# Kernel tuning notes

Hardware: AMD Instinct MI355X
Metric: run time of the kernel (lower is better)

## Reference

```python
import jax, jax.numpy as jnp
import numpy as np

# Module config (matches init_kwargs)
DIM = 1024
NUM_HEADS = 16
HEAD_DIM = DIM // NUM_HEADS
SCALE = HEAD_DIM ** -0.5
WINDOW = 256
EXT = WINDOW // 2  # overlap_window=True -> ext_size = window_size // 2

B, N = 4, 4096  # N is a multiple of WINDOW


def setup_inputs() -> dict:
    key = jax.random.key(0)
    ks = jax.random.split(key, 5)
    x = jax.random.normal(ks[0], (B, N, DIM), dtype=jnp.float32)
    # Learned params (trunc-normal std=0.02 in torch; plain normal*0.02 is fine as a stand-in)
    w_qkv = jax.random.normal(ks[1], (3 * DIM, DIM), dtype=jnp.float32) * 0.02
    b_qkv = jnp.zeros((3 * DIM,), dtype=jnp.float32)
    w_proj = jax.random.normal(ks[2], (DIM, DIM), dtype=jnp.float32) * 0.02
    b_proj = jnp.zeros((DIM,), dtype=jnp.float32)
    return {"x": x, "w_qkv": w_qkv, "b_qkv": b_qkv, "w_proj": w_proj, "b_proj": b_proj}


def _local_attention(x, w_qkv, b_qkv, w_proj, b_proj):
    b, n, c = x.shape
    h, hd, w, e = NUM_HEADS, HEAD_DIM, WINDOW, EXT
    g = n // w  # number of windows (n is a multiple of w)
    kw_len = w + 2 * e  # extended window length for keys/values

    # qkv projection and head split: (3, b, h, n, hd)
    qkv = (x @ w_qkv.T + b_qkv).reshape(b, n, 3, h, hd).transpose(2, 0, 3, 1, 4)
    q, k, v = qkv[0], qkv[1], qkv[2]

    # q: non-overlapping windows -> (b, h, g, w, hd)
    qw = q.reshape(b, h, g, w, hd)

    # k, v: pad seq by ext on both sides, then strided overlapping windows
    kp = jnp.pad(k, ((0, 0), (0, 0), (e, e), (0, 0)))
    vp = jnp.pad(v, ((0, 0), (0, 0), (e, e), (0, 0)))
    # window g covers padded positions [g*w, g*w + kw_len)
    idx = jnp.arange(g)[:, None] * w + jnp.arange(kw_len)[None, :]  # (g, kw_len)
    kw = kp[:, :, idx]  # (b, h, g, kw_len, hd)
    vw = vp[:, :, idx]

    # per-window attention
    dots = jnp.einsum('bhgqd,bhgkd->bhgqk', qw, kw) * SCALE  # (b, h, g, w, kw_len)
    # mask out keys that came from the ext padding (out of [0, n) range)
    pos = idx - e  # global key positions per window
    valid = (pos >= 0) & (pos < n)  # (g, kw_len)
    dots = jnp.where(valid[None, None, :, None, :], dots, -jnp.inf)
    attn = jax.nn.softmax(dots, axis=-1)
    out = jnp.einsum('bhgqk,bhgkd->bhgqd', attn, vw)  # (b, h, g, w, hd)

    # merge windows and heads: (b, n, c)
    out = out.reshape(b, h, n, hd).transpose(0, 2, 1, 3).reshape(b, n, c)
    return out @ w_proj.T + b_proj


def reference(x, w_qkv, b_qkv, w_proj, b_proj):
    return _local_attention(x, w_qkv, b_qkv, w_proj, b_proj)
```

## Files before the change

### kernel.cpp

```cpp
#include <hip/hip_runtime.h>


typedef __attribute__((ext_vector_type(8))) short short8;
typedef __attribute__((ext_vector_type(4))) float f32x4;
typedef __attribute__((ext_vector_type(8))) unsigned short ushort8v;
typedef __attribute__((ext_vector_type(4))) unsigned short ushort4v;
typedef __attribute__((ext_vector_type(4))) unsigned int uint4v;
typedef __attribute__((ext_vector_type(4))) _Float16 half4;

#define K_DIM 1024

__device__ __forceinline__ unsigned short f2bf(float f) {
  unsigned int u = __builtin_bit_cast(unsigned int, f);
  u += 0x7FFFu + ((u >> 16) & 1u);
  return (unsigned short)(u >> 16);
}
__device__ __forceinline__ unsigned short f2h(float f) {
  _Float16 h = (_Float16)f;
  return __builtin_bit_cast(unsigned short, h);
}
__device__ __forceinline__ void gload_lds(const unsigned short* g, unsigned short* l) {
  __builtin_amdgcn_global_load_lds((const __attribute__((address_space(1))) void*)g,
                                   (__attribute__((address_space(3))) void*)l, 16, 0, 0);
}

__global__ __launch_bounds__(256) void convf2b(const float* __restrict__ src,
                                               unsigned short* __restrict__ dst, int n4) {
  int i = blockIdx.x * blockDim.x + threadIdx.x;
  if (i >= n4) return;
  f32x4 v = *(const f32x4*)(src + (size_t)i * 4);
  ushort4v o;
  o[0] = f2bf(v[0]); o[1] = f2bf(v[1]); o[2] = f2bf(v[2]); o[3] = f2bf(v[3]);
  *(ushort4v*)(dst + (size_t)i * 4) = o;
}

__device__ __forceinline__ void gemm_core(const unsigned short* __restrict__ A,
                                          const unsigned short* __restrict__ Bw,
                                          unsigned short* As, unsigned short* Bs,
                                          int m0, int f0, int tid, f32x4 acc[4][4]) {
  const int lane = tid & 63;
  const int w = tid >> 6;
  const int wm = (tid >> 7) & 1;
  const int wn = (tid >> 6) & 1;
  const int q15 = lane & 15, quad = lane >> 4;
  const int sw = q15 & 3;
  for (int kk = 0; kk < K_DIM; kk += 32) {
#pragma unroll
    for (int r = 0; r < 2; ++r) {
      int c = tid + r * 256;
      int row = c >> 2, s = c & 3;
      int gs = s ^ (row & 3);
      const unsigned short* ga = A + (size_t)(m0 + row) * K_DIM + kk + gs * 8;
      const unsigned short* gb = Bw + (size_t)(f0 + row) * K_DIM + kk + gs * 8;
      unsigned short* la = As + (size_t)(w * 64 + r * 256) * 8;
      unsigned short* lb = Bs + (size_t)(w * 64 + r * 256) * 8;
      gload_lds(ga, la);
      gload_lds(gb, lb);
    }
    __syncthreads();
    short8 af[4], bf[4];
#pragma unroll
    for (int i = 0; i < 4; ++i)
      af[i] = *(const short8*)&As[(wm * 64 + i * 16 + q15) * 32 + (quad ^ sw) * 8];
#pragma unroll
    for (int j = 0; j < 4; ++j)
      bf[j] = *(const short8*)&Bs[(wn * 64 + j * 16 + q15) * 32 + (quad ^ sw) * 8];
#pragma unroll
    for (int i = 0; i < 4; ++i)
#pragma unroll
      for (int j = 0; j < 4; ++j)
        acc[i][j] = __builtin_amdgcn_mfma_f32_16x16x32_bf16(af[i], bf[j], acc[i][j], 0, 0, 0);
    __syncthreads();
  }
}

__global__ __launch_bounds__(256) void gemm_qkv(const unsigned short* __restrict__ A,
                                                const unsigned short* __restrict__ Bw,
                                                const float* __restrict__ bias,
                                                unsigned short* __restrict__ q,
                                                unsigned short* __restrict__ k,
                                                unsigned short* __restrict__ v) {
  __shared__ unsigned short As[128 * 32];
  __shared__ unsigned short Bs[128 * 32];
  int m0 = (blockIdx.x & 127) * 128;
  int f0 = (blockIdx.x >> 7) * 128;
  int tid = threadIdx.x;
  f32x4 acc[4][4] = {};
  gemm_core(A, Bw, As, Bs, m0, f0, tid, acc);
  int lane = tid & 63;
  int wm = (tid >> 7) & 1, wn = (tid >> 6) & 1;
  int which = f0 >> 10;
  unsigned short* dst = (which == 0) ? q : ((which == 1) ? k : v);
#pragma unroll
  for (int j = 0; j < 4; ++j) {
    int f = f0 + wn * 64 + j * 16 + (lane & 15);
    int hh = (f >> 6) & 15;
    int d = f & 63;
    float bj = bias[f];
#pragma unroll
    for (int i = 0; i < 4; ++i) {
#pragma unroll
      for (int r = 0; r < 4; ++r) {
        int m = m0 + wm * 64 + i * 16 + (lane >> 4) * 4 + r;
        int bb = m >> 12, n = m & 4095;
        float val = acc[i][j][r] + bj;
        dst[((size_t)(bb * 16 + hh) * 4096 + n) * 64 + d] =
            (which == 2) ? f2h(val) : f2bf(val);
      }
    }
  }
}

__global__ __launch_bounds__(256) void gemm_proj(const unsigned short* __restrict__ A,
                                                 const unsigned short* __restrict__ Bw,
                                                 const float* __restrict__ bias,
                                                 float* __restrict__ out) {
  __shared__ unsigned short As[128 * 32];
  __shared__ unsigned short Bs[128 * 32];
  int m0 = (blockIdx.x & 127) * 128;
  int f0 = (blockIdx.x >> 7) * 128;
  int tid = threadIdx.x;
  f32x4 acc[4][4] = {};
  gemm_core(A, Bw, As, Bs, m0, f0, tid, acc);
  int lane = tid & 63;
  int wm = (tid >> 7) & 1, wn = (tid >> 6) & 1;
#pragma unroll
  for (int j = 0; j < 4; ++j) {
    int f = f0 + wn * 64 + j * 16 + (lane & 15);
    float bj = bias[f];
#pragma unroll
    for (int i = 0; i < 4; ++i) {
#pragma unroll
      for (int r = 0; r < 4; ++r) {
        int m = m0 + wm * 64 + i * 16 + (lane >> 4) * 4 + r;
        out[(size_t)m * 1024 + f] = acc[i][j][r] + bj;
      }
    }
  }
}

__global__ __launch_bounds__(256) void transpose_v(const unsigned short* __restrict__ v,
                                                   unsigned short* __restrict__ vt) {
  __shared__ unsigned short tile[64][72];
  int bid = blockIdx.x;
  int bh = bid >> 6;
  int n0 = (bid & 63) * 64;
  int tid = threadIdx.x;
#pragma unroll
  for (int r = 0; r < 2; ++r) {
    int c = tid + r * 256;
    int row = c >> 3, col8 = (c & 7) * 8;
    uint4v dv = *(const uint4v*)&v[((size_t)bh * 4096 + n0 + row) * 64 + col8];
    *(uint4v*)&tile[row][col8] = dv;
  }
  __syncthreads();
#pragma unroll
  for (int r = 0; r < 2; ++r) {
    int c = tid + r * 256;
    int d = c >> 3, n8 = (c & 7) * 8;
    ushort8v o;
#pragma unroll
    for (int ii = 0; ii < 8; ++ii) o[ii] = tile[n8 + ii][d];
    *(ushort8v*)&vt[((size_t)bh * 64 + d) * 4096 + n0 + n8] = o;
  }
}

__global__ __launch_bounds__(256) void attn3(const unsigned short* __restrict__ Q,
                                             const unsigned short* __restrict__ Kb,
                                             const unsigned short* __restrict__ Vt,
                                             unsigned short* __restrict__ Ao) {
  __shared__ unsigned short lds2[2][8192];

  int bid = blockIdx.x;
  int qb = bid & 63;
  int bh = bid >> 6;
  int b = bh >> 4, h = bh & 15;
  int tid = threadIdx.x, lane = tid & 63, w = tid >> 6;
  int q0 = qb * 64 + w * 16;
  int g = qb >> 2;
  int kst = g * 256 - 128;
  const size_t base = (size_t)bh * 4096 * 64;
  const int q15 = lane & 15, quad = lane >> 4;

  short8 bq[2];
#pragma unroll
  for (int s = 0; s < 2; ++s)
    bq[s] = *(const short8*)&Q[base + (size_t)(q0 + q15) * 64 + s * 32 + quad * 8];

  half4 spk[32];
  float mx = -1e30f;

  auto stageK = [&](int c, int buf) {
    int kb = kst + c * 128;
    kb = min(max(kb, 0), 4096 - 128);
    const unsigned short* Kg = Kb + base + (size_t)kb * 64;
#pragma unroll
    for (int i = 0; i < 4; ++i) {
      int slot = tid + i * 256;
      int row = slot >> 3, s = slot & 7;
      int gs = s ^ (row & 7);
      gload_lds(Kg + (size_t)row * 64 + gs * 8, &lds2[buf][(w * 64 + i * 256) * 8]);
    }
  };

  stageK(0, 0);
#pragma unroll
  for (int c = 0; c < 4; ++c) {
    __syncthreads();
    if (c < 3) stageK(c + 1, (c + 1) & 1);
    const unsigned short* Kc = lds2[c & 1];
    int r7 = q15 & 7;
#pragma unroll
    for (int nt = 0; nt < 8; ++nt) {
      int t = c * 8 + nt;
      int ky = kst + c * 128 + nt * 16;
      bool valid = (ky >= 0) && (ky < 4096);
      if (valid) {
        int sg0 = quad ^ r7;
        const unsigned short* kr = &Kc[(nt * 16 + q15) * 64];
        short8 ak0 = *(const short8*)&kr[sg0 * 8];
        short8 ak1 = *(const short8*)&kr[(sg0 ^ 4) * 8];
        f32x4 sa = {0.f, 0.f, 0.f, 0.f};
        sa = __builtin_amdgcn_mfma_f32_16x16x32_bf16(ak0, bq[0], sa, 0, 0, 0);
        sa = __builtin_amdgcn_mfma_f32_16x16x32_bf16(ak1, bq[1], sa, 0, 0, 0);
        float s0 = sa[0] * 0.125f, s1 = sa[1] * 0.125f;
        float s2 = sa[2] * 0.125f, s3 = sa[3] * 0.125f;
        mx = fmaxf(mx, fmaxf(fmaxf(s0, s1), fmaxf(s2, s3)));
        half4 pk;
        pk[0] = (_Float16)s0; pk[1] = (_Float16)s1;
        pk[2] = (_Float16)s2; pk[3] = (_Float16)s3;
        spk[t] = pk;
      } else {
        spk[t] = (half4){(_Float16)0.f, (_Float16)0.f, (_Float16)0.f, (_Float16)0.f};
      }
    }
  }
  mx = fmaxf(mx, __shfl_xor(mx, 16, 64));
  mx = fmaxf(mx, __shfl_xor(mx, 32, 64));

  auto stageV = [&](int c, int buf) {
    int kb = kst + c * 128;
    kb = min(max(kb, 0), 4096 - 128);
    const unsigned short* Vg = Vt + (size_t)bh * 64 * 4096 + kb;
#pragma unroll
    for (int i = 0; i < 4; ++i) {
      int slot = tid + i * 256;
      int d = slot >> 4, s = slot & 15;
      int gs = s ^ (d & 15);
      gload_lds(Vg + (size_t)d * 4096 + gs * 8, &lds2[buf][(w * 64 + i * 256) * 8]);
    }
  };

  float sum = 0.f;
  f32x4 oacc[4];
#pragma unroll
  for (int dt = 0; dt < 4; ++dt) oacc[dt] = (f32x4){0.f, 0.f, 0.f, 0.f};

  stageV(0, 0);
#pragma unroll
  for (int c = 0; c < 4; ++c) {
    __syncthreads();
    if (c < 3) stageV(c + 1, (c + 1) & 1);
    const unsigned short* Vc = lds2[c & 1];
#pragma unroll
    for (int nt = 0; nt < 8; ++nt) {
      int t = c * 8 + nt;
      int ky = kst + c * 128 + nt * 16;
      bool valid = (ky >= 0) && (ky < 4096);
      if (!valid) continue;
      half4 sp = spk[t];
      float p0 = __expf((float)sp[0] - mx);
      float p1 = __expf((float)sp[1] - mx);
      float p2 = __expf((float)sp[2] - mx);
      float p3 = __expf((float)sp[3] - mx);
      sum += (p0 + p1) + (p2 + p3);
      half4 pk;
      pk[0] = (_Float16)p0; pk[1] = (_Float16)p1;
      pk[2] = (_Float16)p2; pk[3] = (_Float16)p3;
      int sgb = 2 * nt + (quad >> 1);
      int eo = (quad & 1) * 4;
#pragma unroll
      for (int dt = 0; dt < 4; ++dt) {
        int d = dt * 16 + q15;
        half4 bv = *(const half4*)&Vc[d * 128 + ((sgb ^ q15) * 8) + eo];
        oacc[dt] = __builtin_amdgcn_mfma_f32_16x16x16f16(pk, bv, oacc[dt], 0, 0, 0);
      }
    }
  }
  sum += __shfl_xor(sum, 16, 64);
  sum += __shfl_xor(sum, 32, 64);
  float linv = 1.0f / sum;

  float li[4];
#pragma unroll
  for (int r = 0; r < 4; ++r) li[r] = __shfl(linv, quad * 4 + r, 64);
#pragma unroll
  for (int dt = 0; dt < 4; ++dt) {
#pragma unroll
    for (int r = 0; r < 4; ++r) {
      float o = oacc[dt][r] * li[r];
      Ao[(size_t)(b * 4096 + q0 + quad * 4 + r) * 1024 + h * 64 + dt * 16 + q15] = f2bf(o);
    }
  }
}

extern "C" void kernel_launch(void* const* d_in, const int* in_sizes, int n_in,
                              void* d_out, int out_size, void* d_ws, size_t ws_size,
                              hipStream_t stream) {
  const float* x = (const float*)d_in[0];
  const float* w_qkv = (const float*)d_in[1];
  const float* b_qkv = (const float*)d_in[2];
  const float* w_proj = (const float*)d_in[3];
  const float* b_proj = (const float*)d_in[4];
  float* out = (float*)d_out;

  unsigned short* ws = (unsigned short*)d_ws;
  unsigned short* xb = ws;
  unsigned short* wqkvb = ws + 16777216;
  unsigned short* wprojb = ws + 19922944;
  unsigned short* qb = ws + 20971520;
  unsigned short* kb = ws + 37748736;
  unsigned short* vb = ws + 54525952;
  unsigned short* attnb = ws + 71303168;
  unsigned short* vtb = xb;

  convf2b<<<16384, 256, 0, stream>>>(x, xb, 16777216 / 4);
  convf2b<<<3072, 256, 0, stream>>>(w_qkv, wqkvb, 3145728 / 4);
  convf2b<<<1024, 256, 0, stream>>>(w_proj, wprojb, 1048576 / 4);
  gemm_qkv<<<128 * 24, 256, 0, stream>>>(xb, wqkvb, b_qkv, qb, kb, vb);
  transpose_v<<<4096, 256, 0, stream>>>(vb, vtb);
  attn3<<<4096, 256, 0, stream>>>(qb, kb, vtb, attnb);
  gemm_proj<<<128 * 8, 256, 0, stream>>>(attnb, wprojb, b_proj, out);
}
```

Baseline: 425.9 us.

## Fuse V transpose into QKV GEMM epilogue with LDS-staged coalesced stores

The QKV GEMM epilogue now stages each 64-row half of the output tile in shared memory and writes Q/K with 16-byte vectorized row stores. V is written directly in transposed (d-major) layout, which removes the separate transpose_v kernel and its extra global round trip. The 1/8 softmax scale is folded into Q at the epilogue, so the attention kernel no longer multiplies the scores. The cost is extra shared memory and barriers in the epilogue, plus a strided LDS gather for the V transpose. Folding the scale into Q before bf16 rounding may also shift numerics slightly.

```diff
diff --git a/kernel.cpp b/kernel.cpp
--- a/kernel.cpp
+++ b/kernel.cpp
@@ -74,14 +74,86 @@
   }
 }
 
+#define ELD 136
+
 __global__ __launch_bounds__(256) void gemm_qkv(const unsigned short* __restrict__ A,
                                                 const unsigned short* __restrict__ Bw,
                                                 const float* __restrict__ bias,
                                                 unsigned short* __restrict__ q,
                                                 unsigned short* __restrict__ k,
-                                                unsigned short* __restrict__ v) {
-  __shared__ unsigned short As[128 * 32];
-  __shared__ unsigned short Bs[128 * 32];
+                                                unsigned short* __restrict__ vt) {
+  __shared__ unsigned short smem[8704];
+  unsigned short* As = smem;
+  unsigned short* Bs = smem + 4096;
+  int m0 = (blockIdx.x & 127) * 128;
+  int f0 = (blockIdx.x >> 7) * 128;
+  int tid = threadIdx.x;
+  f32x4 acc[4][4] = {};
+  gemm_core(A, Bw, As, Bs, m0, f0, tid, acc);
+
+  int lane = tid & 63;
+  int q15 = lane & 15, quad = lane >> 4;
+  int wm = (tid >> 7) & 1, wn = (tid >> 6) & 1;
+  int which = f0 >> 10;
+  unsigned short* dst = (which == 0) ? q : k;
+  unsigned short* E = smem;
+  int bb = m0 >> 12;
+
+#pragma unroll
+  for (int half = 0; half < 2; ++half) {
+    __syncthreads();
+    if (wm == half) {
+#pragma unroll
+      for (int j = 0; j < 4; ++j) {
+        int col = wn * 64 + j * 16 + q15;
+        float bj = bias[f0 + col];
+#pragma unroll
+        for (int i = 0; i < 4; ++i)
+#pragma unroll
+          for (int r = 0; r < 4; ++r) {
+            float val = acc[i][j][r] + bj;
+            if (which == 0) val *= 0.125f;
+            E[(i * 16 + quad * 4 + r) * ELD + col] =
+                (which == 2) ? f2h(val) : f2bf(val);
+          }
+      }
+    }
+    __syncthreads();
+    if (which != 2) {
+      int lr = tid >> 2, cs = (tid & 3) * 32;
+      int m = m0 + half * 64 + lr;
+      int n = m & 4095;
+      int fg = f0 + cs;
+      int hh = (fg >> 6) & 15, d0 = fg & 63;
+      unsigned short* dp = dst + ((size_t)(bb * 16 + hh) * 4096 + n) * 64 + d0;
+      const unsigned short* ep = &E[lr * ELD + cs];
+#pragma unroll
+      for (int ci = 0; ci < 4; ++ci)
+        *(ushort8v*)(dp + ci * 8) = *(const ushort8v*)(ep + ci * 8);
+    } else {
+      int f = tid >> 1, nseg = (tid & 1) * 32;
+      int fg = f0 + f;
+      int hh = (fg >> 6) & 15, d = fg & 63;
+      int n0g = (m0 & 4095) + half * 64 + nseg;
+      ushort8v o[4];
+#pragma unroll
+      for (int jj = 0; jj < 32; ++jj)
+        o[jj >> 3][jj & 7] = E[(nseg + jj) * ELD + f];
+      unsigned short* vp = vt + ((size_t)(bb * 16 + hh) * 64 + d) * 4096 + n0g;
+#pragma unroll
+      for (int ci = 0; ci < 4; ++ci)
+        *(ushort8v*)(vp + ci * 8) = o[ci];
+    }
+  }
+}
+
+__global__ __launch_bounds__(256) void gemm_proj(const unsigned short* __restrict__ A,
+                                                 const unsigned short* __restrict__ Bw,
+                                                 const float* __restrict__ bias,
+                                                 float* __restrict__ out) {
+  __shared__ unsigned short smem[8192];
+  unsigned short* As = smem;
+  unsigned short* Bs = smem + 4096;
   int m0 = (blockIdx.x & 127) * 128;
   int f0 = (blockIdx.x >> 7) * 128;
   int tid = threadIdx.x;
@@ -89,41 +161,6 @@
   gemm_core(A, Bw, As, Bs, m0, f0, tid, acc);
   int lane = tid & 63;
   int wm = (tid >> 7) & 1, wn = (tid >> 6) & 1;
-  int which = f0 >> 10;
-  unsigned short* dst = (which == 0) ? q : ((which == 1) ? k : v);
-#pragma unroll
-  for (int j = 0; j < 4; ++j) {
-    int f = f0 + wn * 64 + j * 16 + (lane & 15);
-    int hh = (f >> 6) & 15;
-    int d = f & 63;
-    float bj = bias[f];
-#pragma unroll
-    for (int i = 0; i < 4; ++i) {
-#pragma unroll
-      for (int r = 0; r < 4; ++r) {
-        int m = m0 + wm * 64 + i * 16 + (lane >> 4) * 4 + r;
-        int bb = m >> 12, n = m & 4095;
-        float val = acc[i][j][r] + bj;
-        dst[((size_t)(bb * 16 + hh) * 4096 + n) * 64 + d] =
-            (which == 2) ? f2h(val) : f2bf(val);
-      }
-    }
-  }
-}
-
-__global__ __launch_bounds__(256) void gemm_proj(const unsigned short* __restrict__ A,
-                                                 const unsigned short* __restrict__ Bw,
-                                                 const float* __restrict__ bias,
-                                                 float* __restrict__ out) {
-  __shared__ unsigned short As[128 * 32];
-  __shared__ unsigned short Bs[128 * 32];
-  int m0 = (blockIdx.x & 127) * 128;
-  int f0 = (blockIdx.x >> 7) * 128;
-  int tid = threadIdx.x;
-  f32x4 acc[4][4] = {};
-  gemm_core(A, Bw, As, Bs, m0, f0, tid, acc);
-  int lane = tid & 63;
-  int wm = (tid >> 7) & 1, wn = (tid >> 6) & 1;
 #pragma unroll
   for (int j = 0; j < 4; ++j) {
     int f = f0 + wn * 64 + j * 16 + (lane & 15);
@@ -136,32 +173,6 @@
         out[(size_t)m * 1024 + f] = acc[i][j][r] + bj;
       }
     }
-  }
-}
-
-__global__ __launch_bounds__(256) void transpose_v(const unsigned short* __restrict__ v,
-                                                   unsigned short* __restrict__ vt) {
-  __shared__ unsigned short tile[64][72];
-  int bid = blockIdx.x;
-  int bh = bid >> 6;
-  int n0 = (bid & 63) * 64;
-  int tid = threadIdx.x;
-#pragma unroll
-  for (int r = 0; r < 2; ++r) {
-    int c = tid + r * 256;
-    int row = c >> 3, col8 = (c & 7) * 8;
-    uint4v dv = *(const uint4v*)&v[((size_t)bh * 4096 + n0 + row) * 64 + col8];
-    *(uint4v*)&tile[row][col8] = dv;
-  }
-  __syncthreads();
-#pragma unroll
-  for (int r = 0; r < 2; ++r) {
-    int c = tid + r * 256;
-    int d = c >> 3, n8 = (c & 7) * 8;
-    ushort8v o;
-#pragma unroll
-    for (int ii = 0; ii < 8; ++ii) o[ii] = tile[n8 + ii][d];
-    *(ushort8v*)&vt[((size_t)bh * 64 + d) * 4096 + n0 + n8] = o;
   }
 }
 
@@ -223,12 +234,10 @@
         f32x4 sa = {0.f, 0.f, 0.f, 0.f};
         sa = __builtin_amdgcn_mfma_f32_16x16x32_bf16(ak0, bq[0], sa, 0, 0, 0);
         sa = __builtin_amdgcn_mfma_f32_16x16x32_bf16(ak1, bq[1], sa, 0, 0, 0);
-        float s0 = sa[0] * 0.125f, s1 = sa[1] * 0.125f;
-        float s2 = sa[2] * 0.125f, s3 = sa[3] * 0.125f;
-        mx = fmaxf(mx, fmaxf(fmaxf(s0, s1), fmaxf(s2, s3)));
+        mx = fmaxf(mx, fmaxf(fmaxf(sa[0], sa[1]), fmaxf(sa[2], sa[3])));
         half4 pk;
-        pk[0] = (_Float16)s0; pk[1] = (_Float16)s1;
-        pk[2] = (_Float16)s2; pk[3] = (_Float16)s3;
+        pk[0] = (_Float16)sa[0]; pk[1] = (_Float16)sa[1];
+        pk[2] = (_Float16)sa[2]; pk[3] = (_Float16)sa[3];
         spk[t] = pk;
       } else {
         spk[t] = (half4){(_Float16)0.f, (_Float16)0.f, (_Float16)0.f, (_Float16)0.f};
@@ -320,15 +329,13 @@
   unsigned short* wprojb = ws + 19922944;
   unsigned short* qb = ws + 20971520;
   unsigned short* kb = ws + 37748736;
-  unsigned short* vb = ws + 54525952;
+  unsigned short* vtb = ws + 54525952;
   unsigned short* attnb = ws + 71303168;
-  unsigned short* vtb = xb;
 
   convf2b<<<16384, 256, 0, stream>>>(x, xb, 16777216 / 4);
   convf2b<<<3072, 256, 0, stream>>>(w_qkv, wqkvb, 3145728 / 4);
   convf2b<<<1024, 256, 0, stream>>>(w_proj, wprojb, 1048576 / 4);
-  gemm_qkv<<<128 * 24, 256, 0, stream>>>(xb, wqkvb, b_qkv, qb, kb, vb);
-  transpose_v<<<4096, 256, 0, stream>>>(vb, vtb);
+  gemm_qkv<<<128 * 24, 256, 0, stream>>>(xb, wqkvb, b_qkv, qb, kb, vtb);
   attn3<<<4096, 256, 0, stream>>>(qb, kb, vtb, attnb);
   gemm_proj<<<128 * 8, 256, 0, stream>>>(attnb, wprojb, b_proj, out);
 }
```

After: 449.6 us. +5.6%, slower.
